# Optimization experiments

Measured on AMD Instinct MI355X. Metric: run time of the kernel, lower is better.

The kernel has to match this reference:

```python
import jax, jax.numpy as jnp
from jax import lax
import numpy as np

N_IN, N_REC, N_OUT = 128, 512, 20
N_T, N_B = 1000, 64
THR = 1.0
DT, TAU_M, TAU_O = 1.0, 20.0, 20.0
B_O = 0.0
ALPHA = float(np.exp(-DT / TAU_M))  # membrane decay
KAPPA = float(np.exp(-DT / TAU_O))  # output decay
GAIN = (0.5, 0.1, 0.5)              # w_init_gain


def _kaiming(key, shape, gain):
    fan_in = shape[1]
    std = float(np.sqrt(2.0 / fan_in))
    return gain * std * jax.random.normal(key, shape, dtype=jnp.float32)


def setup_inputs() -> dict:
    key = jax.random.key(0)
    k1, k2, k3, k4, k5 = jax.random.split(key, 5)
    x = jax.random.uniform(k1, (N_B, N_T, N_IN), dtype=jnp.float32)
    yt = jax.random.uniform(k2, (N_B, N_T, N_OUT), dtype=jnp.float32)
    w_in = _kaiming(k3, (N_REC, N_IN), GAIN[0])
    w_rec = _kaiming(k4, (N_REC, N_REC), GAIN[1])
    w_out = _kaiming(k5, (N_OUT, N_REC), GAIN[2])
    return {"x": x, "yt": yt, "w_in": w_in, "w_rec": w_rec, "w_out": w_out}


def reference(x, yt, w_in, w_rec, w_out):
    # zero self-recurrence, as in forward(): w_rec *= (1 - eye)
    w_rec_m = w_rec * (1.0 - jnp.eye(N_REC, dtype=w_rec.dtype))

    def step(carry, x_t):
        v, z, vo = carry  # (n_b, n_rec), (n_b, n_rec), (n_b, n_out)
        v_new = ALPHA * v + z @ w_rec_m.T + x_t @ w_in.T - z * THR
        z_new = (v_new > THR).astype(v_new.dtype)
        vo_new = KAPPA * vo + z_new @ w_out.T + B_O
        return (v_new, z_new, vo_new), vo_new

    v0 = jnp.zeros((N_B, N_REC), dtype=x.dtype)
    z0 = jnp.zeros((N_B, N_REC), dtype=x.dtype)
    vo0 = jnp.zeros((N_B, N_OUT), dtype=x.dtype)
    # loop runs t = 0 .. n_t-2, consuming x[:, t, :]
    xs = jnp.swapaxes(x, 0, 1)[: N_T - 1]  # (n_t-1, n_b, n_in)
    _, vo_traj = lax.scan(step, (v0, z0, vo0), xs)
    vo = jnp.concatenate([vo0[None], vo_traj], axis=0)  # (n_t, n_b, n_out), vo[0]=0
    # classif=True: softmax over output units after permute -> (n_b, n_t, n_out)
    yo = jax.nn.softmax(jnp.swapaxes(vo, 0, 1), axis=2)
    return yo
```

## Files before the change

### kernel.cpp

```cpp
#include <hip/hip_runtime.h>
#include <cstdint>
#include <cstddef>

#define N_IN   128
#define N_REC  512
#define N_OUT  20
#define N_T    1000
#define N_B    64
#define NSTEP  999
#define ALPHA_F 0.95122945308685302734375f
#define KAPPA_F 0.95122945308685302734375f

typedef unsigned long long ull;

#define OFF_WINT   0ull
#define OFF_WRECT  262144ull
#define OFF_ZMASK  1312768ull
#define OFF_U      5404672ull
#define OFF_XPROJ  10519552ull
#define NEED_PRE   (OFF_XPROJ + 130940928ull)

__device__ __forceinline__ void bar_lgkm() {
  asm volatile("s_waitcnt lgkmcnt(0)" ::: "memory");
  __builtin_amdgcn_s_barrier();
}

__global__ __launch_bounds__(256) void k_setup(
    const float* __restrict__ w_in, const float* __restrict__ w_rec,
    float* __restrict__ w_inT, float* __restrict__ w_recT) {
  int idx = blockIdx.x * 256 + threadIdx.x;
  if (idx < N_IN * N_REC) {
    int k = idx >> 9, i = idx & 511;
    w_inT[idx] = w_in[i * N_IN + k];
  } else if (idx < N_IN * N_REC + 513 * N_REC) {
    int r = idx - N_IN * N_REC;
    int j = r >> 9, i = r & 511;
    w_recT[r] = (j < N_REC && i != j) ? w_rec[i * N_REC + j] : 0.0f;
  }
}

__global__ __launch_bounds__(256) void k_xprojE(
    const float* __restrict__ x, const float* __restrict__ w_inT,
    float* __restrict__ xproj) {
  __shared__ float xs[32][N_IN];
  int tid = threadIdx.x;
  int R0 = blockIdx.x * 32;
  #pragma unroll
  for (int u = 0; u < 4; ++u) {
    int id = tid + u * 256;
    int rr = id >> 5, c = id & 31;
    int s = R0 + rr;
    int b = s / NSTEP, t = s - b * NSTEP;
    float4 xv = ((const float4*)x)[(size_t)(b * N_T + t) * 32 + c];
    xs[rr][4 * c]     = xv.x;
    xs[rr][4 * c + 1] = xv.y;
    xs[rr][4 * c + 2] = xv.z;
    xs[rr][4 * c + 3] = xv.w;
  }
  __syncthreads();
  float acc[32][2];
  #pragma unroll
  for (int r = 0; r < 32; ++r) { acc[r][0] = 0.f; acc[r][1] = 0.f; }
  for (int k = 0; k < N_IN; ++k) {
    float wa = w_inT[k * N_REC + tid];
    float wb = w_inT[k * N_REC + tid + 256];
    #pragma unroll
    for (int r = 0; r < 32; ++r) {
      acc[r][0] = fmaf(xs[r][k], wa, acc[r][0]);
      acc[r][1] = fmaf(xs[r][k], wb, acc[r][1]);
    }
  }
  #pragma unroll
  for (int r = 0; r < 32; ++r) {
    size_t o0 = (size_t)(R0 + r) * N_REC + tid;
    xproj[o0]       = acc[r][0];
    xproj[o0 + 256] = acc[r][1];
  }
}

struct F16R { float f[16]; };

__device__ __forceinline__ void gload16(F16R& r, const int* __restrict__ L,
                                        int base, const float* __restrict__ wrecp) {
  int4 i0 = *(const int4*)(L + base);
  int4 i1 = *(const int4*)(L + base + 4);
  int4 i2 = *(const int4*)(L + base + 8);
  int4 i3 = *(const int4*)(L + base + 12);
  r.f[0]  = wrecp[(size_t)i0.x << 9];
  r.f[1]  = wrecp[(size_t)i0.y << 9];
  r.f[2]  = wrecp[(size_t)i0.z << 9];
  r.f[3]  = wrecp[(size_t)i0.w << 9];
  r.f[4]  = wrecp[(size_t)i1.x << 9];
  r.f[5]  = wrecp[(size_t)i1.y << 9];
  r.f[6]  = wrecp[(size_t)i1.z << 9];
  r.f[7]  = wrecp[(size_t)i1.w << 9];
  r.f[8]  = wrecp[(size_t)i2.x << 9];
  r.f[9]  = wrecp[(size_t)i2.y << 9];
  r.f[10] = wrecp[(size_t)i2.z << 9];
  r.f[11] = wrecp[(size_t)i2.w << 9];
  r.f[12] = wrecp[(size_t)i3.x << 9];
  r.f[13] = wrecp[(size_t)i3.y << 9];
  r.f[14] = wrecp[(size_t)i3.z << 9];
  r.f[15] = wrecp[(size_t)i3.w << 9];
}

__device__ __forceinline__ float add16(float rec, const F16R& r) {
  #pragma unroll
  for (int u = 0; u < 16; ++u) rec = __fadd_rn(rec, r.f[u]);
  return rec;
}

template <bool PRE>
__global__ __launch_bounds__(512) void k_scanE(
    const float* __restrict__ xproj, const float* __restrict__ x,
    const float* __restrict__ w_inT, const float* __restrict__ w_recT,
    ull* __restrict__ zmask) {
  __shared__ __align__(16) int list[512];
  __shared__ __align__(16) int wcnt_sh[8];
  __shared__ float xrow[2][N_IN];
  int tid = threadIdx.x, b = blockIdx.x;
  int lane = tid & 63, wave = tid >> 6;
  float v = 0.f, z = 0.f;
  int nb = 0;
  float xcur = 0.f;
  if (PRE) {
    xcur = xproj[(size_t)(b * NSTEP) * N_REC + tid];
  } else {
    if (tid < N_IN) xrow[0][tid] = x[(size_t)(b * N_T) * N_IN + tid];
  }
  __syncthreads();
  const float* wrecp = w_recT + tid;
  for (int t = 0; t < NSTEP; ++t) {
    float xnext = 0.f;
    if (PRE) {
      if (t + 1 < NSTEP)
        xnext = xproj[(size_t)(b * NSTEP + t + 1) * N_REC + tid];
    } else {
      if (tid < N_IN && t + 1 < NSTEP)
        xrow[(t + 1) & 1][tid] = x[((size_t)b * N_T + t + 1) * N_IN + tid];
    }
    float xin;
    if (PRE) {
      xin = xcur;
    } else {
      xin = 0.f;
      const float* xr = xrow[t & 1];
      for (int k = 0; k < N_IN; ++k)
        xin = fmaf(xr[k], w_inT[k * N_REC + tid], xin);
    }
    float rec = 0.f;
    {
      F16R A, B2, C;
      if (nb > 0) gload16(A,  list, 0,  wrecp);
      if (nb > 1) gload16(B2, list, 16, wrecp);
      if (nb > 2) gload16(C,  list, 32, wrecp);
      int k = 0;
      while (k < nb) {
        rec = add16(rec, A);
        if (k + 3 < nb) gload16(A, list, (k + 3) << 4, wrecp);
        ++k; if (k >= nb) break;
        rec = add16(rec, B2);
        if (k + 3 < nb) gload16(B2, list, (k + 3) << 4, wrecp);
        ++k; if (k >= nb) break;
        rec = add16(rec, C);
        if (k + 3 < nb) gload16(C, list, (k + 3) << 4, wrecp);
        ++k;
      }
    }
    float t1 = __fmul_rn(ALPHA_F, v);
    t1 = __fadd_rn(t1, rec);
    t1 = __fadd_rn(t1, xin);
    v  = __fsub_rn(t1, z);
    int on = v > 1.0f;
    z = on ? 1.0f : 0.0f;
    ull mask = __ballot(on);
    if (lane == 0) zmask[((size_t)b * NSTEP + t) * 8 + wave] = mask;
    bar_lgkm();
    if (lane == 0) wcnt_sh[wave] = __popcll(mask);
    bar_lgkm();
    int base = 0, ntot = 0;
    #pragma unroll
    for (int w = 0; w < 8; ++w) {
      int cw = wcnt_sh[w];
      if (w < wave) base += cw;
      ntot += cw;
    }
    if (on) {
      int pc = __popcll(mask & ((1ull << lane) - 1));
      list[base + pc] = tid;
    }
    int np16 = (ntot + 15) & ~15;
    if (tid >= ntot && tid < np16) list[tid] = 512;
    bar_lgkm();
    nb = np16 >> 4;
    xcur = xnext;
  }
}

__global__ __launch_bounds__(256) void k_U(
    const ull* __restrict__ zmask, const float* __restrict__ w_out,
    float* __restrict__ U) {
  __shared__ float wT[N_REC][N_OUT];
  int tid = threadIdx.x;
  for (int e = tid; e < N_REC * N_OUT; e += 256) {
    int j = e / N_OUT, o = e - j * N_OUT;
    wT[j][o] = w_out[o * N_REC + j];
  }
  __syncthreads();
  int n = blockIdx.x * 256 + tid;
  if (n >= N_B * NSTEP) return;
  ull m[8];
  #pragma unroll
  for (int w = 0; w < 8; ++w) m[w] = zmask[(size_t)n * 8 + w];
  float acc[N_OUT];
  #pragma unroll
  for (int o = 0; o < N_OUT; ++o) acc[o] = 0.f;
  #pragma unroll
  for (int w = 0; w < 8; ++w) {
    ull bits = m[w];
    while (bits) {
      int j = __builtin_ctzll(bits);
      bits &= bits - 1;
      const float4* r4 = (const float4*)&wT[(w << 6) + j][0];
      float4 r0 = r4[0], r1 = r4[1], r2 = r4[2], r3 = r4[3], r4v = r4[4];
      acc[0]  += r0.x;  acc[1]  += r0.y;  acc[2]  += r0.z;  acc[3]  += r0.w;
      acc[4]  += r1.x;  acc[5]  += r1.y;  acc[6]  += r1.z;  acc[7]  += r1.w;
      acc[8]  += r2.x;  acc[9]  += r2.y;  acc[10] += r2.z;  acc[11] += r2.w;
      acc[12] += r3.x;  acc[13] += r3.y;  acc[14] += r3.z;  acc[15] += r3.w;
      acc[16] += r4v.x; acc[17] += r4v.y; acc[18] += r4v.z; acc[19] += r4v.w;
    }
  }
  float4* Up = (float4*)(U + (size_t)n * N_OUT);
  Up[0] = make_float4(acc[0],  acc[1],  acc[2],  acc[3]);
  Up[1] = make_float4(acc[4],  acc[5],  acc[6],  acc[7]);
  Up[2] = make_float4(acc[8],  acc[9],  acc[10], acc[11]);
  Up[3] = make_float4(acc[12], acc[13], acc[14], acc[15]);
  Up[4] = make_float4(acc[16], acc[17], acc[18], acc[19]);
}

__global__ __launch_bounds__(256) void k_voscan(
    const float* __restrict__ U, float* __restrict__ out) {
  int n = blockIdx.x * 256 + threadIdx.x;
  if (n >= N_B * N_OUT) return;
  int b = n / N_OUT, o = n - b * N_OUT;
  out[(size_t)(b * N_T) * N_OUT + o] = 0.f;
  float acc = 0.f;
  #pragma unroll 9
  for (int t = 0; t < NSTEP; ++t) {
    acc = __fadd_rn(__fmul_rn(KAPPA_F, acc),
                    U[(size_t)(b * NSTEP + t) * N_OUT + o]);
    out[(size_t)(b * N_T + t + 1) * N_OUT + o] = acc;
  }
}

__global__ __launch_bounds__(256) void k_softmax(float* __restrict__ out) {
  int n = blockIdx.x * 256 + threadIdx.x;
  if (n >= N_B * N_T) return;
  float* p = out + (size_t)n * N_OUT;
  float vals[N_OUT];
  #pragma unroll
  for (int o = 0; o < N_OUT; ++o) vals[o] = p[o];
  float mx = vals[0];
  #pragma unroll
  for (int o = 1; o < N_OUT; ++o) mx = fmaxf(mx, vals[o]);
  float s = 0.f;
  #pragma unroll
  for (int o = 0; o < N_OUT; ++o) { vals[o] = expf(vals[o] - mx); s += vals[o]; }
  float inv = 1.0f / s;
  #pragma unroll
  for (int o = 0; o < N_OUT; ++o) p[o] = vals[o] * inv;
}

extern "C" void kernel_launch(void* const* d_in, const int* in_sizes, int n_in,
                              void* d_out, int out_size, void* d_ws, size_t ws_size,
                              hipStream_t stream) {
  int ix = -1, iwin = -1, iwrec = -1, iwout = -1;
  for (int i = 0; i < n_in; ++i) {
    long long s = in_sizes[i];
    if (s == (long long)N_B * N_T * N_IN) ix = i;
    else if (s == N_REC * N_IN)  iwin = i;
    else if (s == N_REC * N_REC) iwrec = i;
    else if (s == N_OUT * N_REC) iwout = i;
  }
  if (ix < 0 || iwin < 0 || iwrec < 0 || iwout < 0) {
    if (n_in >= 5) { ix = 0; iwin = 2; iwrec = 3; iwout = 4; }
    else           { ix = 0; iwin = 1; iwrec = 2; iwout = 3; }
  }
  const float* x     = (const float*)d_in[ix];
  const float* w_in  = (const float*)d_in[iwin];
  const float* w_rec = (const float*)d_in[iwrec];
  const float* w_out = (const float*)d_in[iwout];
  float* out = (float*)d_out;
  char* ws = (char*)d_ws;

  float* w_inT  = (float*)(ws + OFF_WINT);
  float* w_recT = (float*)(ws + OFF_WRECT);
  ull*   zmask  = (ull*)(ws + OFF_ZMASK);
  float* U      = (float*)(ws + OFF_U);
  float* xproj  = (float*)(ws + OFF_XPROJ);

  k_setup<<<1282, 256, 0, stream>>>(w_in, w_rec, w_inT, w_recT);
  if (ws_size >= NEED_PRE) {
    k_xprojE<<<1998, 256, 0, stream>>>(x, w_inT, xproj);
    k_scanE<true><<<N_B, 512, 0, stream>>>(xproj, x, w_inT, w_recT, zmask);
  } else {
    k_scanE<false><<<N_B, 512, 0, stream>>>(xproj, x, w_inT, w_recT, zmask);
  }
  k_U<<<250, 256, 0, stream>>>(zmask, w_out, U);
  k_voscan<<<5, 256, 0, stream>>>(U, out);
  k_softmax<<<250, 256, 0, stream>>>(out);
}
```

Before: 2.507 ms.

## Double-buffer spike list, prefetch indices, precompute byte offsets, retile xproj and voscan

The scan kernel now double-buffers the active-spike list and shares the raw ballot masks instead of per-wave counts, which removes one barrier per timestep. Spike-list indices are stored as precomputed byte offsets and loaded one stage ahead of the gathered w_rec values in a four-deep rotation, taking LDS index loads off the gather critical path. The input-projection kernel processes 48 rows per block instead of 32, and voscan uses 64-thread blocks to spread its 1280 threads over more CUs. The deeper pipeline and larger accumulator array raise register pressure.

```diff
diff --git a/kernel.cpp b/kernel.cpp
--- a/kernel.cpp
+++ b/kernel.cpp
@@ -19,6 +19,8 @@
 #define OFF_U      5404672ull
 #define OFF_XPROJ  10519552ull
 #define NEED_PRE   (OFF_XPROJ + 130940928ull)
+
+#define SENT_OFF   (512 << 11)
 
 __device__ __forceinline__ void bar_lgkm() {
   asm volatile("s_waitcnt lgkmcnt(0)" ::: "memory");
@@ -39,14 +41,15 @@
   }
 }
 
+#define XROWS 48
 __global__ __launch_bounds__(256) void k_xprojE(
     const float* __restrict__ x, const float* __restrict__ w_inT,
     float* __restrict__ xproj) {
-  __shared__ float xs[32][N_IN];
+  __shared__ float xs[XROWS][N_IN];
   int tid = threadIdx.x;
-  int R0 = blockIdx.x * 32;
-  #pragma unroll
-  for (int u = 0; u < 4; ++u) {
+  int R0 = blockIdx.x * XROWS;
+  #pragma unroll
+  for (int u = 0; u < 6; ++u) {
     int id = tid + u * 256;
     int rr = id >> 5, c = id & 31;
     int s = R0 + rr;
@@ -58,20 +61,20 @@
     xs[rr][4 * c + 3] = xv.w;
   }
   __syncthreads();
-  float acc[32][2];
-  #pragma unroll
-  for (int r = 0; r < 32; ++r) { acc[r][0] = 0.f; acc[r][1] = 0.f; }
+  float acc[XROWS][2];
+  #pragma unroll
+  for (int r = 0; r < XROWS; ++r) { acc[r][0] = 0.f; acc[r][1] = 0.f; }
   for (int k = 0; k < N_IN; ++k) {
     float wa = w_inT[k * N_REC + tid];
     float wb = w_inT[k * N_REC + tid + 256];
     #pragma unroll
-    for (int r = 0; r < 32; ++r) {
+    for (int r = 0; r < XROWS; ++r) {
       acc[r][0] = fmaf(xs[r][k], wa, acc[r][0]);
       acc[r][1] = fmaf(xs[r][k], wb, acc[r][1]);
     }
   }
   #pragma unroll
-  for (int r = 0; r < 32; ++r) {
+  for (int r = 0; r < XROWS; ++r) {
     size_t o0 = (size_t)(R0 + r) * N_REC + tid;
     xproj[o0]       = acc[r][0];
     xproj[o0 + 256] = acc[r][1];
@@ -79,29 +82,33 @@
 }
 
 struct F16R { float f[16]; };
-
-__device__ __forceinline__ void gload16(F16R& r, const int* __restrict__ L,
-                                        int base, const float* __restrict__ wrecp) {
-  int4 i0 = *(const int4*)(L + base);
-  int4 i1 = *(const int4*)(L + base + 4);
-  int4 i2 = *(const int4*)(L + base + 8);
-  int4 i3 = *(const int4*)(L + base + 12);
-  r.f[0]  = wrecp[(size_t)i0.x << 9];
-  r.f[1]  = wrecp[(size_t)i0.y << 9];
-  r.f[2]  = wrecp[(size_t)i0.z << 9];
-  r.f[3]  = wrecp[(size_t)i0.w << 9];
-  r.f[4]  = wrecp[(size_t)i1.x << 9];
-  r.f[5]  = wrecp[(size_t)i1.y << 9];
-  r.f[6]  = wrecp[(size_t)i1.z << 9];
-  r.f[7]  = wrecp[(size_t)i1.w << 9];
-  r.f[8]  = wrecp[(size_t)i2.x << 9];
-  r.f[9]  = wrecp[(size_t)i2.y << 9];
-  r.f[10] = wrecp[(size_t)i2.z << 9];
-  r.f[11] = wrecp[(size_t)i2.w << 9];
-  r.f[12] = wrecp[(size_t)i3.x << 9];
-  r.f[13] = wrecp[(size_t)i3.y << 9];
-  r.f[14] = wrecp[(size_t)i3.z << 9];
-  r.f[15] = wrecp[(size_t)i3.w << 9];
+struct I16  { int4 a, b, c, d; };
+
+__device__ __forceinline__ void iload16(I16& r, const int* __restrict__ L, int base) {
+  r.a = *(const int4*)(L + base);
+  r.b = *(const int4*)(L + base + 4);
+  r.c = *(const int4*)(L + base + 8);
+  r.d = *(const int4*)(L + base + 12);
+}
+
+__device__ __forceinline__ void gload16i(F16R& r, const I16& I,
+                                         const char* __restrict__ wb, int t4) {
+  r.f[0]  = *(const float*)(wb + (uint32_t)(I.a.x + t4));
+  r.f[1]  = *(const float*)(wb + (uint32_t)(I.a.y + t4));
+  r.f[2]  = *(const float*)(wb + (uint32_t)(I.a.z + t4));
+  r.f[3]  = *(const float*)(wb + (uint32_t)(I.a.w + t4));
+  r.f[4]  = *(const float*)(wb + (uint32_t)(I.b.x + t4));
+  r.f[5]  = *(const float*)(wb + (uint32_t)(I.b.y + t4));
+  r.f[6]  = *(const float*)(wb + (uint32_t)(I.b.z + t4));
+  r.f[7]  = *(const float*)(wb + (uint32_t)(I.b.w + t4));
+  r.f[8]  = *(const float*)(wb + (uint32_t)(I.c.x + t4));
+  r.f[9]  = *(const float*)(wb + (uint32_t)(I.c.y + t4));
+  r.f[10] = *(const float*)(wb + (uint32_t)(I.c.z + t4));
+  r.f[11] = *(const float*)(wb + (uint32_t)(I.c.w + t4));
+  r.f[12] = *(const float*)(wb + (uint32_t)(I.d.x + t4));
+  r.f[13] = *(const float*)(wb + (uint32_t)(I.d.y + t4));
+  r.f[14] = *(const float*)(wb + (uint32_t)(I.d.z + t4));
+  r.f[15] = *(const float*)(wb + (uint32_t)(I.d.w + t4));
 }
 
 __device__ __forceinline__ float add16(float rec, const F16R& r) {
@@ -115,11 +122,13 @@
     const float* __restrict__ xproj, const float* __restrict__ x,
     const float* __restrict__ w_inT, const float* __restrict__ w_recT,
     ull* __restrict__ zmask) {
-  __shared__ __align__(16) int list[512];
-  __shared__ __align__(16) int wcnt_sh[8];
+  __shared__ __align__(16) int list[2][512];
+  __shared__ ull zbuf[2][8];
   __shared__ float xrow[2][N_IN];
   int tid = threadIdx.x, b = blockIdx.x;
   int lane = tid & 63, wave = tid >> 6;
+  int t4 = tid << 2;
+  const char* wb = (const char*)w_recT;
   float v = 0.f, z = 0.f;
   int nb = 0;
   float xcur = 0.f;
@@ -129,8 +138,9 @@
     if (tid < N_IN) xrow[0][tid] = x[(size_t)(b * N_T) * N_IN + tid];
   }
   __syncthreads();
-  const float* wrecp = w_recT + tid;
   for (int t = 0; t < NSTEP; ++t) {
+    int p = t & 1, q = p ^ 1;
+    const int* L = list[p];
     float xnext = 0.f;
     if (PRE) {
       if (t + 1 < NSTEP)
@@ -150,20 +160,32 @@
     }
     float rec = 0.f;
     {
-      F16R A, B2, C;
-      if (nb > 0) gload16(A,  list, 0,  wrecp);
-      if (nb > 1) gload16(B2, list, 16, wrecp);
-      if (nb > 2) gload16(C,  list, 32, wrecp);
+      I16 I0, I1, I2, I3;
+      F16R D0, D1, D2, D3;
+      if (nb > 0) iload16(I0, L, 0);
+      if (nb > 1) iload16(I1, L, 16);
+      if (nb > 2) iload16(I2, L, 32);
+      if (nb > 0) gload16i(D0, I0, wb, t4);
+      if (nb > 1) gload16i(D1, I1, wb, t4);
+      if (nb > 2) gload16i(D2, I2, wb, t4);
+      if (nb > 3) iload16(I3, L, 48);
       int k = 0;
       while (k < nb) {
-        rec = add16(rec, A);
-        if (k + 3 < nb) gload16(A, list, (k + 3) << 4, wrecp);
+        rec = add16(rec, D0);
+        if (k + 3 < nb) gload16i(D3, I3, wb, t4);
+        if (k + 4 < nb) iload16(I0, L, (k + 4) << 4);
         ++k; if (k >= nb) break;
-        rec = add16(rec, B2);
-        if (k + 3 < nb) gload16(B2, list, (k + 3) << 4, wrecp);
+        rec = add16(rec, D1);
+        if (k + 3 < nb) gload16i(D0, I0, wb, t4);
+        if (k + 4 < nb) iload16(I1, L, (k + 4) << 4);
         ++k; if (k >= nb) break;
-        rec = add16(rec, C);
-        if (k + 3 < nb) gload16(C, list, (k + 3) << 4, wrecp);
+        rec = add16(rec, D2);
+        if (k + 3 < nb) gload16i(D1, I1, wb, t4);
+        if (k + 4 < nb) iload16(I2, L, (k + 4) << 4);
+        ++k; if (k >= nb) break;
+        rec = add16(rec, D3);
+        if (k + 3 < nb) gload16i(D2, I2, wb, t4);
+        if (k + 4 < nb) iload16(I3, L, (k + 4) << 4);
         ++k;
       }
     }
@@ -174,23 +196,25 @@
     int on = v > 1.0f;
     z = on ? 1.0f : 0.0f;
     ull mask = __ballot(on);
-    if (lane == 0) zmask[((size_t)b * NSTEP + t) * 8 + wave] = mask;
-    bar_lgkm();
-    if (lane == 0) wcnt_sh[wave] = __popcll(mask);
+    if (lane == 0) {
+      zmask[((size_t)b * NSTEP + t) * 8 + wave] = mask;
+      zbuf[q][wave] = mask;
+    }
     bar_lgkm();
     int base = 0, ntot = 0;
     #pragma unroll
     for (int w = 0; w < 8; ++w) {
-      int cw = wcnt_sh[w];
-      if (w < wave) base += cw;
-      ntot += cw;
+      ull mw = zbuf[q][w];
+      int c = __popcll(mw);
+      if (w < wave) base += c;
+      ntot += c;
     }
     if (on) {
       int pc = __popcll(mask & ((1ull << lane) - 1));
-      list[base + pc] = tid;
+      list[q][base + pc] = tid << 11;
     }
     int np16 = (ntot + 15) & ~15;
-    if (tid >= ntot && tid < np16) list[tid] = 512;
+    if (tid >= ntot && tid < np16) list[q][tid] = SENT_OFF;
     bar_lgkm();
     nb = np16 >> 4;
     xcur = xnext;
@@ -238,9 +262,9 @@
   Up[4] = make_float4(acc[16], acc[17], acc[18], acc[19]);
 }
 
-__global__ __launch_bounds__(256) void k_voscan(
+__global__ __launch_bounds__(64) void k_voscan(
     const float* __restrict__ U, float* __restrict__ out) {
-  int n = blockIdx.x * 256 + threadIdx.x;
+  int n = blockIdx.x * 64 + threadIdx.x;
   if (n >= N_B * N_OUT) return;
   int b = n / N_OUT, o = n - b * N_OUT;
   out[(size_t)(b * N_T) * N_OUT + o] = 0.f;
@@ -301,12 +325,12 @@
 
   k_setup<<<1282, 256, 0, stream>>>(w_in, w_rec, w_inT, w_recT);
   if (ws_size >= NEED_PRE) {
-    k_xprojE<<<1998, 256, 0, stream>>>(x, w_inT, xproj);
+    k_xprojE<<<1332, 256, 0, stream>>>(x, w_inT, xproj);
     k_scanE<true><<<N_B, 512, 0, stream>>>(xproj, x, w_inT, w_recT, zmask);
   } else {
     k_scanE<false><<<N_B, 512, 0, stream>>>(xproj, x, w_inT, w_recT, zmask);
   }
   k_U<<<250, 256, 0, stream>>>(zmask, w_out, U);
-  k_voscan<<<5, 256, 0, stream>>>(U, out);
+  k_voscan<<<20, 64, 0, stream>>>(U, out);
   k_softmax<<<250, 256, 0, stream>>>(out);
 }
```

Result: faster. 2.277 ms (-9.2%).
